# Optimization experiments

Hardware: AMD Instinct MI355X
Metric: run time of the kernel (lower is better)

Reference implementation:

```python
import jax, jax.numpy as jnp
import numpy as np

NUM_TOKENS = 1048576
NUM_EXPERTS = 64


def setup_inputs() -> dict:
    key = jax.random.key(0)
    router_logits_fp32 = jax.random.normal(key, (NUM_TOKENS, NUM_EXPERTS), dtype=jnp.float32)
    return {"router_logits_fp32": router_logits_fp32, "top_k": 8}


def reference(router_logits_fp32, top_k):
    # Fused softmax over experts + top-k selection (aiter.topk_softmax with renorm=True).
    probs = jax.nn.softmax(router_logits_fp32, axis=-1)          # [T, E]
    topk_weights, topk_ids = jax.lax.top_k(probs, top_k)         # [T, K], [T, K]
    # renormalize selected weights to sum to 1 per token (the trailing True flag)
    topk_weights = topk_weights / jnp.sum(topk_weights, axis=-1, keepdims=True)
    num_tokens = router_logits_fp32.shape[0]
    # token_expert_indices[t, k] = t * top_k + k (row-major source-row mapping used
    # later for the token permutation/scatter into expert buffers)
    token_expert_indices = jnp.arange(num_tokens * top_k, dtype=jnp.int32).reshape(num_tokens, top_k)
    return topk_weights, topk_ids.astype(jnp.int32), token_expert_indices
```

## Files before the change

kernel.cpp:

```cpp
#include <hip/hip_runtime.h>
#include <stdint.h>


typedef float  f32x4 __attribute__((ext_vector_type(4)));

#define DPP_QUAD_XOR1   0xB1
#define DPP_QUAD_XOR2   0x4E
#define DPP_HALF_MIRROR 0x141

template<int CTRL>
static __device__ __forceinline__ uint64_t dpp64(uint64_t x) {
    int lo = __builtin_amdgcn_update_dpp(0, (int)(uint32_t)x,         CTRL, 0xF, 0xF, true);
    int hi = __builtin_amdgcn_update_dpp(0, (int)(uint32_t)(x >> 32), CTRL, 0xF, 0xF, true);
    return ((uint64_t)(uint32_t)hi << 32) | (uint32_t)lo;
}

template<int CTRL>
static __device__ __forceinline__ float dppf(float x) {
    int i = __builtin_amdgcn_update_dpp(0, __float_as_int(x), CTRL, 0xF, 0xF, true);
    return __int_as_float(i);
}

static __device__ __forceinline__ uint64_t make_key(float v, int c) {
    uint32_t u = __float_as_uint(v);
    uint32_t o = (u & 0x80000000u) ? ~u : (u | 0x80000000u);
    return ((uint64_t)o << 6) | (uint32_t)c;
}

__global__ __launch_bounds__(256) void topk_softmax_k(
    const float* __restrict__ logits,
    float* __restrict__ out_w,
    float* __restrict__ out_id,
    float* __restrict__ out_tei,
    int T)
{
    const int  lane = threadIdx.x & 63;
    const int  wv   = (int)(threadIdx.x >> 6);
    const long t0   = (long)blockIdx.x * 32 + (long)wv * 8;
    if (t0 >= T) return;

    const int  tok_in_grp = lane >> 3;
    const int  sub        = lane & 7;
    const bool act        = (t0 + tok_in_grp) < T;

    const f32x4* src = reinterpret_cast<const f32x4*>(logits)
                     + (act ? (t0 * 16 + (long)lane * 2) : 0);
    f32x4 a = __builtin_nontemporal_load(src);
    f32x4 b = __builtin_nontemporal_load(src + 1);

    const int cb = 63 - sub * 8;
    uint64_t k0 = make_key(a.x, cb    );
    uint64_t k1 = make_key(a.y, cb - 1);
    uint64_t k2 = make_key(a.z, cb - 2);
    uint64_t k3 = make_key(a.w, cb - 3);
    uint64_t k4 = make_key(b.x, cb - 4);
    uint64_t k5 = make_key(b.y, cb - 5);
    uint64_t k6 = make_key(b.z, cb - 6);
    uint64_t k7 = make_key(b.w, cb - 7);

#define CE(x, y) { if (x < y) { uint64_t t_ = x; x = y; y = t_; } }
    CE(k0,k1) CE(k2,k3) CE(k4,k5) CE(k6,k7)
    CE(k0,k2) CE(k1,k3) CE(k4,k6) CE(k5,k7)
    CE(k1,k2) CE(k5,k6)
    CE(k0,k4) CE(k1,k5) CE(k2,k6) CE(k3,k7)
    CE(k2,k4) CE(k3,k5)
    CE(k1,k2) CE(k3,k4) CE(k5,k6)
#undef CE

    uint64_t mykey = 0;
    uint64_t mtop  = 0;
#pragma unroll
    for (int k = 0; k < 8; ++k) {
        uint64_t w = k0;
        { uint64_t o = dpp64<DPP_QUAD_XOR1>(w);   if (o > w) w = o; }
        { uint64_t o = dpp64<DPP_QUAD_XOR2>(w);   if (o > w) w = o; }
        { uint64_t o = dpp64<DPP_HALF_MIRROR>(w); if (o > w) w = o; }
        if (k == 0) mtop = w;
        if (sub == k) mykey = w;
        if (k0 == w) {
            k0 = k1; k1 = k2; k2 = k3; k3 = k4;
            k4 = k5; k5 = k6; k6 = k7; k7 = 0;
        }
    }

    uint32_t o  = (uint32_t)(mykey >> 6);
    uint32_t ub = (o & 0x80000000u) ? (o & 0x7fffffffu) : ~o;
    float    v  = __uint_as_float(ub);
    int      idx = 63 - (int)(mykey & 63);

    uint32_t om = (uint32_t)(mtop >> 6);
    uint32_t mb = (om & 0x80000000u) ? (om & 0x7fffffffu) : ~om;
    float    mv = __uint_as_float(mb);

    float e = __expf(v - mv);
    float s = e;
    s += dppf<DPP_QUAD_XOR1>(s);
    s += dppf<DPP_QUAD_XOR2>(s);
    s += dppf<DPP_HALF_MIRROR>(s);
    float wgt = e / s;

    if (act) {
        const long oi = t0 * 8 + lane;
        __builtin_nontemporal_store(wgt,        &out_w[oi]);
        __builtin_nontemporal_store((float)idx, &out_id[oi]);
        __builtin_nontemporal_store((float)oi,  &out_tei[oi]);
    }
}

extern "C" void kernel_launch(void* const* d_in, const int* in_sizes, int n_in,
                              void* d_out, int out_size, void* d_ws, size_t ws_size,
                              hipStream_t stream) {
    const float* logits = (const float*)d_in[0];
    const int T = in_sizes[0] / 64;

    float* outw = (float*)d_out;
    float* outi = outw + (size_t)T * 8;
    float* outt = outi + (size_t)T * 8;

    const int blocks = (T + 31) / 32;
    hipLaunchKernelGGL(topk_softmax_k, dim3(blocks), dim3(256), 0, stream,
                       logits, outw, outi, outt, T);
}
```

Before: 83.72 us.

## Replace iterative top-k extraction with bitonic DPP merge on double-encoded keys

Encodes each order-preserving key plus column index as a double, so compare-exchange becomes fmax/fmin instead of 64-bit integer compares. The serial eight-round max-extract across lanes is replaced by three bitonic merge levels, each using DPP lane exchanges and a small sorting network. The final division becomes a hardware reciprocal multiply. It depends on f64 min/max throughput and on the fractional index bits staying exact in a double, and it adds more DPP traffic per level.

After: 78.12 us. -6.7%, faster.

```diff
diff --git a/kernel.cpp b/kernel.cpp
--- a/kernel.cpp
+++ b/kernel.cpp
@@ -2,17 +2,19 @@
 #include <stdint.h>
 
 
-typedef float  f32x4 __attribute__((ext_vector_type(4)));
+typedef float f32x4 __attribute__((ext_vector_type(4)));
 
 #define DPP_QUAD_XOR1   0xB1
 #define DPP_QUAD_XOR2   0x4E
 #define DPP_HALF_MIRROR 0x141
 
 template<int CTRL>
-static __device__ __forceinline__ uint64_t dpp64(uint64_t x) {
-    int lo = __builtin_amdgcn_update_dpp(0, (int)(uint32_t)x,         CTRL, 0xF, 0xF, true);
-    int hi = __builtin_amdgcn_update_dpp(0, (int)(uint32_t)(x >> 32), CTRL, 0xF, 0xF, true);
-    return ((uint64_t)(uint32_t)hi << 32) | (uint32_t)lo;
+static __device__ __forceinline__ double dpp64d(double x) {
+    uint64_t b = (uint64_t)__double_as_longlong(x);
+    int lo = __builtin_amdgcn_update_dpp(0, (int)(uint32_t)b,         CTRL, 0xF, 0xF, true);
+    int hi = __builtin_amdgcn_update_dpp(0, (int)(uint32_t)(b >> 32), CTRL, 0xF, 0xF, true);
+    uint64_t r = ((uint64_t)(uint32_t)hi << 32) | (uint32_t)lo;
+    return __longlong_as_double((long long)r);
 }
 
 template<int CTRL>
@@ -21,10 +23,21 @@
     return __int_as_float(i);
 }
 
-static __device__ __forceinline__ uint64_t make_key(float v, int c) {
-    uint32_t u = __float_as_uint(v);
-    uint32_t o = (u & 0x80000000u) ? ~u : (u | 0x80000000u);
-    return ((uint64_t)o << 6) | (uint32_t)c;
+#define CED(x, y) { double hi_ = fmax(x, y), lo_ = fmin(x, y); x = hi_; y = lo_; }
+
+template<int CTRL>
+static __device__ __forceinline__ void merge_level(double k[8]) {
+    double m[8];
+#pragma unroll
+    for (int i = 0; i < 8; ++i) {
+        double p = dpp64d<CTRL>(k[7 - i]);
+        m[i] = fmax(k[i], p);
+    }
+    CED(m[0], m[4]) CED(m[1], m[5]) CED(m[2], m[6]) CED(m[3], m[7])
+    CED(m[0], m[2]) CED(m[1], m[3]) CED(m[4], m[6]) CED(m[5], m[7])
+    CED(m[0], m[1]) CED(m[2], m[3]) CED(m[4], m[5]) CED(m[6], m[7])
+#pragma unroll
+    for (int i = 0; i < 8; ++i) k[i] = m[i];
 }
 
 __global__ __launch_bounds__(256) void topk_softmax_k(
@@ -39,65 +52,61 @@
     const long t0   = (long)blockIdx.x * 32 + (long)wv * 8;
     if (t0 >= T) return;
 
-    const int  tok_in_grp = lane >> 3;
-    const int  sub        = lane & 7;
-    const bool act        = (t0 + tok_in_grp) < T;
+    const int  sub = lane & 7;
+    const bool act = (t0 + (lane >> 3)) < T;
 
     const f32x4* src = reinterpret_cast<const f32x4*>(logits)
                      + (act ? (t0 * 16 + (long)lane * 2) : 0);
     f32x4 a = __builtin_nontemporal_load(src);
     f32x4 b = __builtin_nontemporal_load(src + 1);
 
-    const int cb = 63 - sub * 8;
-    uint64_t k0 = make_key(a.x, cb    );
-    uint64_t k1 = make_key(a.y, cb - 1);
-    uint64_t k2 = make_key(a.z, cb - 2);
-    uint64_t k3 = make_key(a.w, cb - 3);
-    uint64_t k4 = make_key(b.x, cb - 4);
-    uint64_t k5 = make_key(b.y, cb - 5);
-    uint64_t k6 = make_key(b.z, cb - 6);
-    uint64_t k7 = make_key(b.w, cb - 7);
+    const float vals[8] = {a.x, a.y, a.z, a.w, b.x, b.y, b.z, b.w};
+    const double base = (double)(63 - sub * 8) * 0.015625;
 
-#define CE(x, y) { if (x < y) { uint64_t t_ = x; x = y; y = t_; } }
-    CE(k0,k1) CE(k2,k3) CE(k4,k5) CE(k6,k7)
-    CE(k0,k2) CE(k1,k3) CE(k4,k6) CE(k5,k7)
-    CE(k1,k2) CE(k5,k6)
-    CE(k0,k4) CE(k1,k5) CE(k2,k6) CE(k3,k7)
-    CE(k2,k4) CE(k3,k5)
-    CE(k1,k2) CE(k3,k4) CE(k5,k6)
-#undef CE
-
-    uint64_t mykey = 0;
-    uint64_t mtop  = 0;
+    double k[8];
 #pragma unroll
-    for (int k = 0; k < 8; ++k) {
-        uint64_t w = k0;
-        { uint64_t o = dpp64<DPP_QUAD_XOR1>(w);   if (o > w) w = o; }
-        { uint64_t o = dpp64<DPP_QUAD_XOR2>(w);   if (o > w) w = o; }
-        { uint64_t o = dpp64<DPP_HALF_MIRROR>(w); if (o > w) w = o; }
-        if (k == 0) mtop = w;
-        if (sub == k) mykey = w;
-        if (k0 == w) {
-            k0 = k1; k1 = k2; k2 = k3; k3 = k4;
-            k4 = k5; k5 = k6; k6 = k7; k7 = 0;
-        }
+    for (int j = 0; j < 8; ++j) {
+        uint32_t u = __float_as_uint(vals[j]);
+        uint32_t o = (u & 0x80000000u) ? ~u : (u | 0x80000000u);
+        k[j] = (double)o + (base - j * 0.015625);
     }
 
-    uint32_t o  = (uint32_t)(mykey >> 6);
-    uint32_t ub = (o & 0x80000000u) ? (o & 0x7fffffffu) : ~o;
-    float    v  = __uint_as_float(ub);
-    int      idx = 63 - (int)(mykey & 63);
+    CED(k[0],k[1]) CED(k[2],k[3]) CED(k[4],k[5]) CED(k[6],k[7])
+    CED(k[0],k[2]) CED(k[1],k[3]) CED(k[4],k[6]) CED(k[5],k[7])
+    CED(k[1],k[2]) CED(k[5],k[6])
+    CED(k[0],k[4]) CED(k[1],k[5]) CED(k[2],k[6]) CED(k[3],k[7])
+    CED(k[2],k[4]) CED(k[3],k[5])
+    CED(k[1],k[2]) CED(k[3],k[4]) CED(k[5],k[6])
 
-    uint32_t om = (uint32_t)(mtop >> 6);
-    uint32_t mb = (om & 0x80000000u) ? (om & 0x7fffffffu) : ~om;
+    merge_level<DPP_QUAD_XOR1>(k);
+    merge_level<DPP_QUAD_XOR2>(k);
+    merge_level<DPP_HALF_MIRROR>(k);
+
+    double t4a = (sub & 4) ? k[4] : k[0];
+    double t4b = (sub & 4) ? k[5] : k[1];
+    double t4c = (sub & 4) ? k[6] : k[2];
+    double t4d = (sub & 4) ? k[7] : k[3];
+    double t2a = (sub & 2) ? t4c : t4a;
+    double t2b = (sub & 2) ? t4d : t4b;
+    double sel = (sub & 1) ? t2b : t2a;
+
+    uint32_t o0 = (uint32_t)k[0];
+    uint32_t mb = (o0 & 0x80000000u) ? (o0 & 0x7fffffffu) : ~o0;
     float    mv = __uint_as_float(mb);
+
+    uint32_t os   = (uint32_t)sel;
+    double   frac = sel - (double)os;
+    int      cidx = (int)(frac * 64.0 + 0.5);
+    int      idx  = 63 - cidx;
+    uint32_t ub   = (os & 0x80000000u) ? (os & 0x7fffffffu) : ~os;
+    float    v    = __uint_as_float(ub);
 
     float e = __expf(v - mv);
     float s = e;
     s += dppf<DPP_QUAD_XOR1>(s);
     s += dppf<DPP_QUAD_XOR2>(s);
     s += dppf<DPP_HALF_MIRROR>(s);
-    float wgt = e / s;
+    float wgt = e * __builtin_amdgcn_rcpf(s);
 
     if (act) {
         const long oi = t0 * 8 + lane;
```
